# Kernel optimization log

Hardware: AMD Instinct MI355X
Metric: run time of the kernel (lower is better)

## Reference

```python
import jax, jax.numpy as jnp
import numpy as np
from functools import partial

# Model constants (from init_kwargs / cell & synapse param dicts)
DT = 1.0
TAU_MEM = 20.0
TAU_REF = 2.0
TAU_SYN = np.array([5.0, 10.0], dtype=np.float32)   # [ampa, gaba]
TAU_SYN_FF = 5.0
SIGNS = np.array([1.0, -1.0], dtype=np.float32)      # exc +, inh -
SURRGRAD_SCALE = 10.0
REF_STEPS = TAU_REF / DT

B, T, NIN, N, S = 16, 500, 1024, 4096, 2


@jax.custom_vjp
def spike_fn(x):
    # Heaviside forward, fast-sigmoid surrogate gradient backward
    return (x > 0).astype(x.dtype)

def _spike_fwd(x):
    return spike_fn(x), x

def _spike_bwd(x, g):
    surr = 1.0 / (SURRGRAD_SCALE * jnp.abs(x) + 1.0) ** 2
    return (g * surr,)

spike_fn.defvjp(_spike_fwd, _spike_bwd)


def setup_inputs() -> dict:
    key = jax.random.key(0)
    k1, k2, k3 = jax.random.split(key, 3)
    input_spikes = (jax.random.uniform(k1, (B, T, NIN)) < 0.05).astype(jnp.float32)
    W = jax.random.uniform(k2, (N, N), dtype=jnp.float32) * 0.01    # positive magnitudes
    W_FF = jax.random.uniform(k3, (NIN, N), dtype=jnp.float32) * 0.05
    cell_type_indices = (jnp.arange(N) >= int(0.8 * N)).astype(jnp.int32)
    return {"input_spikes": input_spikes, "W": W, "W_FF": W_FF,
            "cell_type_indices": cell_type_indices}


def _simulate(input_spikes, W, W_FF, cell_type_indices):
    beta = jnp.float32(np.exp(-DT / TAU_MEM))
    alpha = jnp.asarray(np.exp(-DT / TAU_SYN), dtype=jnp.float32)   # [S]
    alpha_ff = jnp.float32(np.exp(-DT / TAU_SYN_FF))
    signs = jnp.asarray(SIGNS)

    # per-synapse-type signed recurrent weights: W_stack [S, N_pre, N_post]
    masks = (cell_type_indices[None, :] == jnp.arange(S)[:, None]).astype(W.dtype)  # [S,N]
    W_stack = signs[:, None, None] * masks[:, :, None] * W[None]

    v0 = jnp.zeros((B, N), jnp.float32)
    I0 = jnp.zeros((B, S, N), jnp.float32)
    Iff0 = jnp.zeros((B, N), jnp.float32)
    ref0 = jnp.zeros((B, N), jnp.float32)
    spk0 = jnp.zeros((B, N), jnp.float32)

    def step(carry, spk_in_t):
        v, I, Iff, ref, spk = carry
        # recurrent drive per synapse type: [B,S,N]
        drive = jnp.einsum('bn,snm->bsm', spk, W_stack)
        I = alpha[None, :, None] * I + drive
        Iff = alpha_ff * Iff + spk_in_t @ W_FF
        I_total = I.sum(axis=1) + Iff
        active = ref <= 0.0
        v_new = jnp.where(active, beta * v + (1.0 - beta) * I_total, 0.0)
        s_new = jnp.where(active, spike_fn(v_new - 1.0), 0.0)
        ref_new = jnp.where(s_new > 0, REF_STEPS, jnp.maximum(ref - 1.0, 0.0))
        v_out = v_new * (1.0 - s_new)   # reset to 0 on spike (natural units)
        return (v_out, I, Iff, ref_new, s_new), s_new

    _, spikes = jax.lax.scan(step, (v0, I0, Iff0, ref0, spk0),
                             jnp.transpose(input_spikes, (1, 0, 2)))  # [T,B,NIN]
    return jnp.transpose(spikes, (1, 0, 2))  # [B,T,N]


def reference(input_spikes, W, W_FF, cell_type_indices):
    return _simulate(input_spikes, W, W_FF, cell_type_indices)
```

## Files before the change

### kernel.cpp

```cpp
#include <hip/hip_runtime.h>
#include <cmath>
#include <cstdint>

typedef unsigned long long u64;
typedef uint16_t u16;
typedef uint32_t u32;

#define NB 16
#define NT 500
#define NINPUT 1024
#define NN 4096
#define NWORDS 64
#define FWORDS 16

#define E_OFF 0
#define I_OFF 3328
#define F_OFF 4192
#define L_TOT 5216

__global__ __launch_bounds__(256) void k_inmask(const float* __restrict__ in, u64* __restrict__ inmask){
  int idx = blockIdx.x * 256 + threadIdx.x;
  u64 bal = __ballot(in[idx] > 0.0f);
  if ((threadIdx.x & 63) == 0) inmask[idx >> 6] = bal;
}

__global__ __launch_bounds__(256) void k_init(float* __restrict__ st, u64* __restrict__ rmask0,
                                              u64* __restrict__ excw, const int* __restrict__ ctype){
  int idx = blockIdx.x * 256 + threadIdx.x;
#pragma unroll
  for (int a = 0; a < 5; ++a) st[(size_t)a * NB * NN + idx] = 0.0f;
  if (idx < NB * NWORDS) rmask0[idx] = 0ull;
  if (idx < NN){
    u64 bal = __ballot(ctype[idx] == 0);
    if ((threadIdx.x & 63) == 0) excw[idx >> 6] = bal;
  }
}

__device__ __forceinline__ float chain_sum(const char* __restrict__ Wc,
                                           const u16* __restrict__ L,
                                           int cnt, u32 m4, u32 rowmask)
{
  float acc = 0.0f;
  if (cnt <= 0) return acc;
  const int nfull = cnt >> 5;
  const int rem   = cnt & 31;
  float wA[32], wB[32], wT[32];

#define LOADF(buf, gb) {                                                    \
    _Pragma("unroll")                                                       \
    for (int q = 0; q < 4; ++q){                                            \
      uint4 pk = *(const uint4*)(L + (gb) + q * 8);                         \
      const u32 wda[4] = {pk.x, pk.y, pk.z, pk.w};                          \
      _Pragma("unroll")                                                     \
      for (int h = 0; h < 4; ++h){                                          \
        const int j0 = q * 8 + h * 2;                                       \
        u32 n0 = wda[h] & 0xFFFFu;                                          \
        u32 n1 = wda[h] >> 16;                                              \
        buf[j0]     = *(const float*)(Wc + ((n0 << 14) + m4));              \
        buf[j0 + 1] = *(const float*)(Wc + ((n1 << 14) + m4));              \
      }                                                                      \
    }                                                                        \
  }

#define ACC32(buf) { _Pragma("unroll") for (int j = 0; j < 32; ++j) acc = __fadd_rn(acc, buf[j]); }

  if (rem){
    const int gb = nfull << 5;
#pragma unroll
    for (int q = 0; q < 4; ++q){
      uint4 pk = *(const uint4*)(L + gb + q * 8);
      const u32 wda[4] = {pk.x, pk.y, pk.z, pk.w};
#pragma unroll
      for (int h = 0; h < 4; ++h){
        const int j0 = q * 8 + h * 2;
        u32 n0 = (j0     < rem) ? (wda[h] & 0xFFFFu & rowmask) : 0u;
        u32 n1 = (j0 + 1 < rem) ? ((wda[h] >> 16) & rowmask)   : 0u;
        float v0 = *(const float*)(Wc + ((n0 << 14) + m4));
        float v1 = *(const float*)(Wc + ((n1 << 14) + m4));
        wT[j0]     = (j0     < rem) ? v0 : 0.0f;
        wT[j0 + 1] = (j0 + 1 < rem) ? v1 : 0.0f;
      }
    }
  }

  if (nfull){
    LOADF(wA, 0)
    int g = 0;
    for (; g + 2 <= nfull; g += 2){
      LOADF(wB, (g + 1) << 5)
      ACC32(wA)
      if (g + 2 < nfull) LOADF(wA, (g + 2) << 5)
      ACC32(wB)
    }
    if (nfull & 1) ACC32(wA)
  }
  if (rem) ACC32(wT)

#undef LOADF
#undef ACC32
  return acc;
}

__global__ __launch_bounds__(256) void k_step(
    const float* __restrict__ W, const float* __restrict__ Wff,
    const u64* __restrict__ excw, const u64* __restrict__ inmask,
    const u64* __restrict__ rcur, u64* __restrict__ rnxt,
    float* __restrict__ v, float* __restrict__ I0, float* __restrict__ I1,
    float* __restrict__ Iff, float* __restrict__ refc, float* __restrict__ out,
    int t, float a0, float a1, float aff, float beta, float omb)
{
  const int lane = threadIdx.x & 63;
  const int wv   = threadIdx.x >> 6;
  const int bk   = blockIdx.x;
  const int chunk = (bk & 7) * 8 + ((bk >> 3) & 7);
  const int b     = (bk >> 6) * 4 + wv;
  const int m     = chunk * 64 + lane;

  __shared__ __align__(16) u16 lst[4][L_TOT];
  u16* Lb = lst[wv];

  u64 bits = rcur[b * NWORDS + lane];
  u64 ew   = excw[lane];
  u64 be = bits & ew;
  u64 bi = bits & ~ew;

  int tot_e, tot_i, tot_f;
  {
    int c = __popcll(be), p = c;
    for (int d = 1; d < 64; d <<= 1){ int o = __shfl_up(p, d, 64); if (lane >= d) p += o; }
    int k = E_OFF + (p - c);
    tot_e = __shfl(p, 63, 64);
    u64 x = be;
    while (x){ int j = __builtin_ctzll(x); x &= x - 1; Lb[k++] = (u16)((lane << 6) | j); }
  }
  {
    int c = __popcll(bi), p = c;
    for (int d = 1; d < 64; d <<= 1){ int o = __shfl_up(p, d, 64); if (lane >= d) p += o; }
    int k = I_OFF + (p - c);
    tot_i = __shfl(p, 63, 64);
    u64 x = bi;
    while (x){ int j = __builtin_ctzll(x); x &= x - 1; Lb[k++] = (u16)((lane << 6) | j); }
  }
  {
    u64 bf = (lane < FWORDS) ? inmask[((size_t)b * NT + t) * FWORDS + lane] : 0ull;
    int c = __popcll(bf), p = c;
    for (int d = 1; d < 64; d <<= 1){ int o = __shfl_up(p, d, 64); if (lane >= d) p += o; }
    int k = F_OFF + (p - c);
    tot_f = __shfl(p, 63, 64);
    u64 x = bf;
    while (x){ int j = __builtin_ctzll(x); x &= x - 1; Lb[k++] = (u16)((lane << 6) | j); }
  }

  const char* Wc  = (const char*)W;
  const char* Wfc = (const char*)Wff;
  const u32 m4 = (u32)(m << 2);

  float de = chain_sum(Wc,  Lb + E_OFF, tot_e, m4, 4095u);
  float di = chain_sum(Wc,  Lb + I_OFF, tot_i, m4, 4095u);
  float df = chain_sum(Wfc, Lb + F_OFF, tot_f, m4, 1023u);

  const int sidx = b * NN + m;
  float i0 = __fadd_rn(__fmul_rn(a0, I0[sidx]), de);
  float i1 = __fadd_rn(__fmul_rn(a1, I1[sidx]), -di);
  float ff = __fadd_rn(__fmul_rn(aff, Iff[sidx]), df);
  float itot = __fadd_rn(__fadd_rn(i0, i1), ff);
  float rv = refc[sidx];
  float vo = v[sidx];
  float vn = (rv <= 0.0f) ? __fadd_rn(__fmul_rn(beta, vo), __fmul_rn(omb, itot)) : 0.0f;
  bool s = vn > 1.0f;
  refc[sidx] = s ? 2.0f : fmaxf(rv - 1.0f, 0.0f);
  v[sidx]    = s ? 0.0f : vn;
  I0[sidx] = i0; I1[sidx] = i1; Iff[sidx] = ff;
  out[(size_t)b * NT * NN + (size_t)t * NN + m] = s ? 1.0f : 0.0f;

  u64 bal = __ballot(s);
  if (lane == 0) rnxt[b * NWORDS + chunk] = bal;
}

extern "C" void kernel_launch(void* const* d_in, const int* in_sizes, int n_in,
                              void* d_out, int out_size, void* d_ws, size_t ws_size,
                              hipStream_t stream)
{
  const float* in_sp = (const float*)d_in[0];
  const float* W     = (const float*)d_in[1];
  const float* Wff   = (const float*)d_in[2];
  const int*   ctype = (const int*)d_in[3];
  float* out = (float*)d_out;

  char* ws = (char*)d_ws;
  float* st = (float*)ws;
  size_t off = (size_t)5 * NB * NN * sizeof(float);
  u64* rm0    = (u64*)(ws + off); off += (size_t)NB * NWORDS * 8;
  u64* rm1    = (u64*)(ws + off); off += (size_t)NB * NWORDS * 8;
  u64* excw   = (u64*)(ws + off); off += (size_t)NWORDS * 8;
  u64* inmask = (u64*)(ws + off); off += (size_t)NB * NT * FWORDS * 8;

  float* v   = st;
  float* I0  = st + (size_t)1 * NB * NN;
  float* I1  = st + (size_t)2 * NB * NN;
  float* Ifp = st + (size_t)3 * NB * NN;
  float* rfp = st + (size_t)4 * NB * NN;

  float af  = -1.0f / 5.0f;
  float bf  = -1.0f / 10.0f;
  float a0  = (float)std::exp((double)af);
  float a1  = (float)std::exp((double)bf);
  float aff = (float)std::exp(-1.0 / 5.0);
  float beta = (float)std::exp(-1.0 / 20.0);
  float omb  = 1.0f - beta;

  k_inmask<<<(NB * NT * NINPUT) / 256, 256, 0, stream>>>(in_sp, inmask);
  k_init<<<(NB * NN) / 256, 256, 0, stream>>>(st, rm0, excw, ctype);

  for (int t = 0; t < NT; ++t){
    const u64* rc = (t & 1) ? rm1 : rm0;
    u64*       rn = (t & 1) ? rm0 : rm1;
    k_step<<<256, 256, 0, stream>>>(W, Wff, excw, inmask, rc, rn,
                                    v, I0, I1, Ifp, rfp, out,
                                    t, a0, a1, aff, beta, omb);
  }
}
```

Before: 18.07 ms.

## Fuse all timesteps into one persistent kernel with a global atomic barrier

Replaces the 500 per-timestep launches with a single persistent kernel of 256 blocks. Blocks synchronise each step through an atomic counter barrier and exchange spike bitmasks through a triple-buffered global array. Neuron state (v, currents, refractory counter) now stays in registers instead of being read and written in global memory every step. The gather loop is rewritten with three rotating buffers, and padded index lists remove the separate remainder path. The main costs removed are launch overhead and state traffic. In exchange, correctness relies on all 256 blocks being co-resident, and each step now pays for a spin-wait grid barrier.

```diff
diff --git a/kernel.cpp b/kernel.cpp
--- a/kernel.cpp
+++ b/kernel.cpp
@@ -3,20 +3,24 @@
 #include <cstdint>
 
 typedef unsigned long long u64;
+typedef uint32_t u32;
 typedef uint16_t u16;
-typedef uint32_t u32;
 
 #define NB 16
 #define NT 500
-#define NINPUT 1024
+#define NIN 1024
 #define NN 4096
 #define NWORDS 64
 #define FWORDS 16
+#define NBLK 256
 
 #define E_OFF 0
+#define E_CAP 3328
 #define I_OFF 3328
-#define F_OFF 4192
-#define L_TOT 5216
+#define I_CAP 896
+#define F_OFF 4224
+#define F_CAP 1056
+#define L_TOT 5280
 
 __global__ __launch_bounds__(256) void k_inmask(const float* __restrict__ in, u64* __restrict__ inmask){
   int idx = blockIdx.x * 256 + threadIdx.x;
@@ -24,90 +28,89 @@
   if ((threadIdx.x & 63) == 0) inmask[idx >> 6] = bal;
 }
 
-__global__ __launch_bounds__(256) void k_init(float* __restrict__ st, u64* __restrict__ rmask0,
+__global__ __launch_bounds__(256) void k_init(u64* __restrict__ rm, u32* __restrict__ barcnt,
                                               u64* __restrict__ excw, const int* __restrict__ ctype){
   int idx = blockIdx.x * 256 + threadIdx.x;
+  if (idx < 3 * NB * NWORDS) rm[idx] = 0ull;
+  if (idx == 0) *barcnt = 0u;
+  u64 bal = __ballot(ctype[idx] == 0);
+  if ((threadIdx.x & 63) == 0) excw[idx >> 6] = bal;
+}
+
+__device__ __forceinline__ int build16(u64 bits, u16* __restrict__ L, int lane){
+  int c = __popcll(bits), p = c;
 #pragma unroll
-  for (int a = 0; a < 5; ++a) st[(size_t)a * NB * NN + idx] = 0.0f;
-  if (idx < NB * NWORDS) rmask0[idx] = 0ull;
-  if (idx < NN){
-    u64 bal = __ballot(ctype[idx] == 0);
-    if ((threadIdx.x & 63) == 0) excw[idx >> 6] = bal;
-  }
-}
-
-__device__ __forceinline__ float chain_sum(const char* __restrict__ Wc,
-                                           const u16* __restrict__ L,
-                                           int cnt, u32 m4, u32 rowmask)
+  for (int d = 1; d < 64; d <<= 1){ int o = __shfl_up(p, d, 64); if (lane >= d) p += o; }
+  int k = p - c;
+  int tot = __shfl(p, 63, 64);
+  u64 x = bits;
+  u32 base = ((u32)lane) << 6;
+  while (x){ int j = __builtin_ctzll(x); x &= x - 1; L[k++] = (u16)(base | (u32)j); }
+  if (lane < 32) L[tot + lane] = 0;
+  return tot;
+}
+
+__device__ __forceinline__ float chain16(const char* __restrict__ Wc,
+                                         const u16* __restrict__ L,
+                                         int cnt, u32 m4)
 {
   float acc = 0.0f;
-  if (cnt <= 0) return acc;
-  const int nfull = cnt >> 5;
-  const int rem   = cnt & 31;
-  float wA[32], wB[32], wT[32];
-
-#define LOADF(buf, gb) {                                                    \
-    _Pragma("unroll")                                                       \
-    for (int q = 0; q < 4; ++q){                                            \
-      uint4 pk = *(const uint4*)(L + (gb) + q * 8);                         \
-      const u32 wda[4] = {pk.x, pk.y, pk.z, pk.w};                          \
-      _Pragma("unroll")                                                     \
-      for (int h = 0; h < 4; ++h){                                          \
-        const int j0 = q * 8 + h * 2;                                       \
-        u32 n0 = wda[h] & 0xFFFFu;                                          \
-        u32 n1 = wda[h] >> 16;                                              \
-        buf[j0]     = *(const float*)(Wc + ((n0 << 14) + m4));              \
-        buf[j0 + 1] = *(const float*)(Wc + ((n1 << 14) + m4));              \
-      }                                                                      \
-    }                                                                        \
+  const int ngrp = (cnt + 31) >> 5;
+  if (ngrp <= 0) return acc;
+  const int rem = cnt & 31;
+  float A[32], B[32], C[32];
+
+#define CS_LOAD(buf, g) { \
+    const uint4* q4_ = (const uint4*)(L + ((g) << 5)); \
+    _Pragma("unroll") \
+    for (int q = 0; q < 4; ++q){ \
+      uint4 pk = q4_[q]; \
+      u32 w0 = pk.x, w1 = pk.y, w2 = pk.z, w3 = pk.w; \
+      buf[q*8+0] = *(const float*)(Wc + (((w0 & 0xFFFFu) << 14) + m4)); \
+      buf[q*8+1] = *(const float*)(Wc + (((w0 >> 16)     << 14) + m4)); \
+      buf[q*8+2] = *(const float*)(Wc + (((w1 & 0xFFFFu) << 14) + m4)); \
+      buf[q*8+3] = *(const float*)(Wc + (((w1 >> 16)     << 14) + m4)); \
+      buf[q*8+4] = *(const float*)(Wc + (((w2 & 0xFFFFu) << 14) + m4)); \
+      buf[q*8+5] = *(const float*)(Wc + (((w2 >> 16)     << 14) + m4)); \
+      buf[q*8+6] = *(const float*)(Wc + (((w3 & 0xFFFFu) << 14) + m4)); \
+      buf[q*8+7] = *(const float*)(Wc + (((w3 >> 16)     << 14) + m4)); \
+    } }
+
+#define CS_ACC(buf, g) { \
+    if ((g) == ngrp - 1 && rem){ \
+      _Pragma("unroll") \
+      for (int j = 0; j < 32; ++j){ float pv_ = (j < rem) ? buf[j] : 0.0f; acc = __fadd_rn(acc, pv_); } \
+    } else { \
+      _Pragma("unroll") \
+      for (int j = 0; j < 32; ++j) acc = __fadd_rn(acc, buf[j]); \
+    } }
+
+  CS_LOAD(A, 0)
+  if (1 < ngrp) CS_LOAD(B, 1)
+  if (2 < ngrp) CS_LOAD(C, 2)
+  int g = 0;
+  for (;;){
+    CS_ACC(A, g)
+    if (g + 3 < ngrp) CS_LOAD(A, g + 3)
+    if (++g == ngrp) break;
+    CS_ACC(B, g)
+    if (g + 3 < ngrp) CS_LOAD(B, g + 3)
+    if (++g == ngrp) break;
+    CS_ACC(C, g)
+    if (g + 3 < ngrp) CS_LOAD(C, g + 3)
+    if (++g == ngrp) break;
   }
-
-#define ACC32(buf) { _Pragma("unroll") for (int j = 0; j < 32; ++j) acc = __fadd_rn(acc, buf[j]); }
-
-  if (rem){
-    const int gb = nfull << 5;
-#pragma unroll
-    for (int q = 0; q < 4; ++q){
-      uint4 pk = *(const uint4*)(L + gb + q * 8);
-      const u32 wda[4] = {pk.x, pk.y, pk.z, pk.w};
-#pragma unroll
-      for (int h = 0; h < 4; ++h){
-        const int j0 = q * 8 + h * 2;
-        u32 n0 = (j0     < rem) ? (wda[h] & 0xFFFFu & rowmask) : 0u;
-        u32 n1 = (j0 + 1 < rem) ? ((wda[h] >> 16) & rowmask)   : 0u;
-        float v0 = *(const float*)(Wc + ((n0 << 14) + m4));
-        float v1 = *(const float*)(Wc + ((n1 << 14) + m4));
-        wT[j0]     = (j0     < rem) ? v0 : 0.0f;
-        wT[j0 + 1] = (j0 + 1 < rem) ? v1 : 0.0f;
-      }
-    }
-  }
-
-  if (nfull){
-    LOADF(wA, 0)
-    int g = 0;
-    for (; g + 2 <= nfull; g += 2){
-      LOADF(wB, (g + 1) << 5)
-      ACC32(wA)
-      if (g + 2 < nfull) LOADF(wA, (g + 2) << 5)
-      ACC32(wB)
-    }
-    if (nfull & 1) ACC32(wA)
-  }
-  if (rem) ACC32(wT)
-
-#undef LOADF
-#undef ACC32
+#undef CS_LOAD
+#undef CS_ACC
   return acc;
 }
 
-__global__ __launch_bounds__(256) void k_step(
+__global__ __launch_bounds__(256) void k_fused(
     const float* __restrict__ W, const float* __restrict__ Wff,
     const u64* __restrict__ excw, const u64* __restrict__ inmask,
-    const u64* __restrict__ rcur, u64* __restrict__ rnxt,
-    float* __restrict__ v, float* __restrict__ I0, float* __restrict__ I1,
-    float* __restrict__ Iff, float* __restrict__ refc, float* __restrict__ out,
-    int t, float a0, float a1, float aff, float beta, float omb)
+    u64* __restrict__ rm, u32* __restrict__ barcnt,
+    float* __restrict__ out,
+    float a0, float a1, float aff, float beta, float omb)
 {
   const int lane = threadIdx.x & 63;
   const int wv   = threadIdx.x >> 6;
@@ -115,66 +118,59 @@
   const int chunk = (bk & 7) * 8 + ((bk >> 3) & 7);
   const int b     = (bk >> 6) * 4 + wv;
   const int m     = chunk * 64 + lane;
+  const u32 m4    = (u32)(m << 2);
 
   __shared__ __align__(16) u16 lst[4][L_TOT];
   u16* Lb = lst[wv];
 
-  u64 bits = rcur[b * NWORDS + lane];
-  u64 ew   = excw[lane];
-  u64 be = bits & ew;
-  u64 bi = bits & ~ew;
-
-  int tot_e, tot_i, tot_f;
-  {
-    int c = __popcll(be), p = c;
-    for (int d = 1; d < 64; d <<= 1){ int o = __shfl_up(p, d, 64); if (lane >= d) p += o; }
-    int k = E_OFF + (p - c);
-    tot_e = __shfl(p, 63, 64);
-    u64 x = be;
-    while (x){ int j = __builtin_ctzll(x); x &= x - 1; Lb[k++] = (u16)((lane << 6) | j); }
-  }
-  {
-    int c = __popcll(bi), p = c;
-    for (int d = 1; d < 64; d <<= 1){ int o = __shfl_up(p, d, 64); if (lane >= d) p += o; }
-    int k = I_OFF + (p - c);
-    tot_i = __shfl(p, 63, 64);
-    u64 x = bi;
-    while (x){ int j = __builtin_ctzll(x); x &= x - 1; Lb[k++] = (u16)((lane << 6) | j); }
-  }
-  {
-    u64 bf = (lane < FWORDS) ? inmask[((size_t)b * NT + t) * FWORDS + lane] : 0ull;
-    int c = __popcll(bf), p = c;
-    for (int d = 1; d < 64; d <<= 1){ int o = __shfl_up(p, d, 64); if (lane >= d) p += o; }
-    int k = F_OFF + (p - c);
-    tot_f = __shfl(p, 63, 64);
-    u64 x = bf;
-    while (x){ int j = __builtin_ctzll(x); x &= x - 1; Lb[k++] = (u16)((lane << 6) | j); }
-  }
-
   const char* Wc  = (const char*)W;
   const char* Wfc = (const char*)Wff;
-  const u32 m4 = (u32)(m << 2);
-
-  float de = chain_sum(Wc,  Lb + E_OFF, tot_e, m4, 4095u);
-  float di = chain_sum(Wc,  Lb + I_OFF, tot_i, m4, 4095u);
-  float df = chain_sum(Wfc, Lb + F_OFF, tot_f, m4, 1023u);
-
-  const int sidx = b * NN + m;
-  float i0 = __fadd_rn(__fmul_rn(a0, I0[sidx]), de);
-  float i1 = __fadd_rn(__fmul_rn(a1, I1[sidx]), -di);
-  float ff = __fadd_rn(__fmul_rn(aff, Iff[sidx]), df);
-  float itot = __fadd_rn(__fadd_rn(i0, i1), ff);
-  float rv = refc[sidx];
-  float vo = v[sidx];
-  float vn = (rv <= 0.0f) ? __fadd_rn(__fmul_rn(beta, vo), __fmul_rn(omb, itot)) : 0.0f;
-  bool s = vn > 1.0f;
-  refc[sidx] = s ? 2.0f : fmaxf(rv - 1.0f, 0.0f);
-  v[sidx]    = s ? 0.0f : vn;
-  I0[sidx] = i0; I1[sidx] = i1; Iff[sidx] = ff;
-  out[(size_t)b * NT * NN + (size_t)t * NN + m] = s ? 1.0f : 0.0f;
-
-  u64 bal = __ballot(s);
-  if (lane == 0) rnxt[b * NWORDS + chunk] = bal;
+  const u64 ew = excw[lane];
+
+  float vv = 0.0f, xi0 = 0.0f, xi1 = 0.0f, xff = 0.0f, rv = 0.0f;
+
+  for (int t = 0; t < NT; ++t){
+    u64* rcur = rm + (size_t)(t % 3)       * (NB * NWORDS);
+    u64* rnxt = rm + (size_t)((t + 1) % 3) * (NB * NWORDS);
+
+    u64 bits = __hip_atomic_load(&rcur[b * NWORDS + lane],
+                                 __ATOMIC_RELAXED, __HIP_MEMORY_SCOPE_AGENT);
+    u64 be = bits & ew;
+    u64 bi = bits & ~ew;
+    u64 bf = (lane < FWORDS) ? inmask[((size_t)b * NT + t) * FWORDS + lane] : 0ull;
+
+    int tot_e = build16(be, Lb + E_OFF, lane);
+    int tot_i = build16(bi, Lb + I_OFF, lane);
+    int tot_f = build16(bf, Lb + F_OFF, lane);
+
+    float de = chain16(Wc,  Lb + E_OFF, tot_e, m4);
+    float di = chain16(Wc,  Lb + I_OFF, tot_i, m4);
+    float df = chain16(Wfc, Lb + F_OFF, tot_f, m4);
+
+    xi0 = __fadd_rn(__fmul_rn(a0,  xi0), de);
+    xi1 = __fadd_rn(__fmul_rn(a1,  xi1), -di);
+    xff = __fadd_rn(__fmul_rn(aff, xff), df);
+    float itot = __fadd_rn(__fadd_rn(xi0, xi1), xff);
+    float vn = (rv <= 0.0f) ? __fadd_rn(__fmul_rn(beta, vv), __fmul_rn(omb, itot)) : 0.0f;
+    bool s = vn > 1.0f;
+    rv = s ? 2.0f : fmaxf(rv - 1.0f, 0.0f);
+    vv = s ? 0.0f : vn;
+    out[(size_t)b * NT * NN + (size_t)t * NN + m] = s ? 1.0f : 0.0f;
+
+    u64 bal = __ballot(s);
+    if (lane == 0)
+      __hip_atomic_store(&rnxt[b * NWORDS + chunk], bal,
+                         __ATOMIC_RELAXED, __HIP_MEMORY_SCOPE_AGENT);
+
+    __syncthreads();
+    if (threadIdx.x == 0){
+      __hip_atomic_fetch_add(barcnt, 1u, __ATOMIC_ACQ_REL, __HIP_MEMORY_SCOPE_AGENT);
+      const u32 target = (u32)(t + 1) * NBLK;
+      while (__hip_atomic_load(barcnt, __ATOMIC_ACQUIRE, __HIP_MEMORY_SCOPE_AGENT) < target)
+        __builtin_amdgcn_s_sleep(1);
+    }
+    __syncthreads();
+  }
 }
 
 extern "C" void kernel_launch(void* const* d_in, const int* in_sizes, int n_in,
@@ -188,18 +184,11 @@
   float* out = (float*)d_out;
 
   char* ws = (char*)d_ws;
-  float* st = (float*)ws;
-  size_t off = (size_t)5 * NB * NN * sizeof(float);
-  u64* rm0    = (u64*)(ws + off); off += (size_t)NB * NWORDS * 8;
-  u64* rm1    = (u64*)(ws + off); off += (size_t)NB * NWORDS * 8;
+  u64* rm     = (u64*)ws;
+  size_t off  = (size_t)3 * NB * NWORDS * 8;
   u64* excw   = (u64*)(ws + off); off += (size_t)NWORDS * 8;
   u64* inmask = (u64*)(ws + off); off += (size_t)NB * NT * FWORDS * 8;
-
-  float* v   = st;
-  float* I0  = st + (size_t)1 * NB * NN;
-  float* I1  = st + (size_t)2 * NB * NN;
-  float* Ifp = st + (size_t)3 * NB * NN;
-  float* rfp = st + (size_t)4 * NB * NN;
+  u32* barcnt = (u32*)(ws + off); off += 64;
 
   float af  = -1.0f / 5.0f;
   float bf  = -1.0f / 10.0f;
@@ -209,14 +198,8 @@
   float beta = (float)std::exp(-1.0 / 20.0);
   float omb  = 1.0f - beta;
 
-  k_inmask<<<(NB * NT * NINPUT) / 256, 256, 0, stream>>>(in_sp, inmask);
-  k_init<<<(NB * NN) / 256, 256, 0, stream>>>(st, rm0, excw, ctype);
-
-  for (int t = 0; t < NT; ++t){
-    const u64* rc = (t & 1) ? rm1 : rm0;
-    u64*       rn = (t & 1) ? rm0 : rm1;
-    k_step<<<256, 256, 0, stream>>>(W, Wff, excw, inmask, rc, rn,
-                                    v, I0, I1, Ifp, rfp, out,
-                                    t, a0, a1, aff, beta, omb);
-  }
-}
+  k_inmask<<<(NB * NT * NIN) / 256, 256, 0, stream>>>(in_sp, inmask);
+  k_init<<<16, 256, 0, stream>>>(rm, barcnt, excw, ctype);
+  k_fused<<<NBLK, 256, 0, stream>>>(W, Wff, excw, inmask, rm, barcnt, out,
+                                    a0, a1, aff, beta, omb);
+}
```

Result: slower. 49.77 ms (+175.4%).
